# Optimization experiments

Hardware: AMD Instinct MI355X
Metric: run time of the kernel (lower is better)

## Reference

```python
import jax, jax.numpy as jnp
import numpy as np

B, S, H = 8, 4096, 1024
E, K = 64, 2
CAP_FACTOR = 1.25
TEMP = 1.0
LBW = 0.01


def setup_inputs() -> dict:
    key = jax.random.key(0)
    k1, k2, k3 = jax.random.split(key, 3)
    x = jax.random.normal(k1, (B, S, H), dtype=jnp.float32)
    gate_w = jax.random.normal(k2, (E, H), dtype=jnp.float32) * 0.02
    expert_w = jax.random.normal(k3, (E, H, H), dtype=jnp.float32) * 0.02
    return {"x": x, "gate_w": gate_w, "expert_w": expert_w}


def _moe_forward(x, gate_w, expert_w):
    b, s, h = x.shape
    xf = x.reshape(-1, h)                      # [N, H]
    N = xf.shape[0]
    capacity = int(N * K / E * CAP_FACTOR)

    # --- gating ---
    logits = xf @ gate_w.T                     # [N, E]
    vals, idx = jax.lax.top_k(logits / TEMP, K)  # [N, K]
    probs = jax.nn.softmax(vals, axis=-1)      # [N, K]

    # --- dispatch: first-come-first-served position within each expert ---
    ef = idx.reshape(-1)                       # [N*K], token-major order (matches torch loop)
    onehot = jax.nn.one_hot(ef, E, dtype=jnp.int32)            # [N*K, E]
    pos = jnp.take_along_axis(jnp.cumsum(onehot, axis=0), ef[:, None], axis=1)[:, 0] - 1
    valid = pos < capacity
    slot = jnp.where(valid, ef * capacity + pos, E * capacity)  # out-of-range -> dropped

    # token_map[e, c] = token_idx * K + k  (or -1 if empty)
    token_map = jnp.full((E * capacity,), -1, dtype=jnp.int32)
    token_map = token_map.at[slot].set(jnp.arange(N * K, dtype=jnp.int32), mode="drop")

    tok = jnp.clip(token_map // K, 0, N - 1)
    filled = token_map >= 0
    expert_inputs = jnp.where(filled[:, None], xf[tok], 0.0)    # [E*cap, H]
    expert_inputs = expert_inputs.reshape(E, capacity, h)

    # --- grouped expert GEMM (no bias; zero rows stay zero) ---
    expert_outputs = jnp.einsum("ech,edh->ecd", expert_inputs, expert_w)  # [E, cap, H]

    # --- combine: weighted scatter-add back to tokens ---
    eo_flat = expert_outputs.reshape(E * capacity, h)
    wk = token_map % K
    weight = jnp.where(filled, probs[tok, jnp.clip(wk, 0, K - 1)], 0.0)
    out_idx = jnp.where(filled, tok, N)        # invalid -> dropped
    output = jnp.zeros((N, h), dtype=xf.dtype).at[out_idx].add(
        weight[:, None] * eo_flat, mode="drop")

    # --- aux load-balancing loss ---
    gate_probs = jax.nn.softmax(logits, axis=-1)
    usage = jnp.bincount(ef, length=E).astype(jnp.float32) / (N * K + 1e-9)
    importance = gate_probs.mean(axis=0)
    aux = jnp.sum(usage * importance) * E
    aux = jnp.minimum(aux * LBW, 1.0)

    return output.reshape(b, s, h), aux


def reference(x, gate_w, expert_w):
    return _moe_forward(x, gate_w, expert_w)
```

## Files before the change

kernel.cpp:

```cpp
#include <hip/hip_runtime.h>
#include <hip/hip_bf16.h>

#define NTOK 32768
#define NE 64
#define HD 1024
#define CAP 1280
#define NKF (NTOK*2)
#define NSLOT (NE*CAP)
#define NTILE 128

typedef __attribute__((ext_vector_type(8))) short bf16x8;
typedef __attribute__((ext_vector_type(4))) short bf16x4;
typedef __attribute__((ext_vector_type(4))) float f32x4;
typedef __attribute__((ext_vector_type(4))) unsigned short u16x4;

__device__ __hip_bfloat16 g_zero[1152];

__device__ __forceinline__ short f2bf(float f) {
  union { __hip_bfloat16 b; short s; } u;
  u.b = __float2bfloat16(f);
  return u.s;
}
__device__ __forceinline__ float bf2f(unsigned short h) {
  return __uint_as_float(((unsigned)h) << 16);
}

__global__ __launch_bounds__(256, 4) void gating_kernel(const float* __restrict__ x,
                                                        const float* __restrict__ gw,
                                                        float* __restrict__ logits,
                                                        __hip_bfloat16* __restrict__ xb,
                                                        const float* __restrict__ ew,
                                                        __hip_bfloat16* __restrict__ wb) {
  __shared__ float Xs[64][66];
  __shared__ float Gs[64][66];
  const int tid = threadIdx.x;
  const int tok0 = blockIdx.x * 64;
  const int th = tid >> 4;
  const int te = tid & 15;
  float acc[4][4];
#pragma unroll
  for (int i = 0; i < 4; ++i)
#pragma unroll
    for (int j = 0; j < 4; ++j) acc[i][j] = 0.f;

  size_t ci = ((size_t)blockIdx.x * 256 + tid) * 8;
  const size_t cstride = (size_t)512 * 256 * 8;

  for (int k0i = 0; k0i < 16; ++k0i) {
    const int k0 = k0i * 64;
#pragma unroll
    for (int r = 0; r < 4; ++r) {
      int idx = r * 256 + tid;
      int row = idx >> 4;
      int c = (idx & 15) * 4;
      float4 xv4 = *(const float4*)&x[(size_t)(tok0 + row) * HD + k0 + c];
      *(float4*)&Xs[row][c] = xv4;
      bf16x4 o;
      o[0] = f2bf(xv4.x); o[1] = f2bf(xv4.y); o[2] = f2bf(xv4.z); o[3] = f2bf(xv4.w);
      *(bf16x4*)&xb[(size_t)(tok0 + row) * HD + k0 + c] = o;
      *(float4*)&Gs[row][c] = *(const float4*)&gw[(size_t)row * HD + k0 + c];
    }
    float4 ca[2], cb[2];
#pragma unroll
    for (int q = 0; q < 2; ++q) {
      ca[q] = *(const float4*)(ew + ci + (size_t)q * cstride);
      cb[q] = *(const float4*)(ew + ci + (size_t)q * cstride + 4);
    }
    __syncthreads();
#pragma unroll 4
    for (int kk = 0; kk < 8; ++kk) {
      float4 xv[4], gv[4];
#pragma unroll
      for (int i = 0; i < 4; ++i) xv[i] = *(float4*)&Xs[th + i * 16][kk * 4];
#pragma unroll
      for (int j = 0; j < 4; ++j) gv[j] = *(float4*)&Gs[te + j * 16][kk * 4];
#pragma unroll
      for (int i = 0; i < 4; ++i)
#pragma unroll
        for (int j = 0; j < 4; ++j) {
          acc[i][j] = fmaf(xv[i].x, gv[j].x, acc[i][j]);
          acc[i][j] = fmaf(xv[i].y, gv[j].y, acc[i][j]);
          acc[i][j] = fmaf(xv[i].z, gv[j].z, acc[i][j]);
          acc[i][j] = fmaf(xv[i].w, gv[j].w, acc[i][j]);
        }
    }
#pragma unroll
    for (int q = 0; q < 2; ++q) {
      bf16x8 o;
      o[0] = f2bf(ca[q].x); o[1] = f2bf(ca[q].y); o[2] = f2bf(ca[q].z); o[3] = f2bf(ca[q].w);
      o[4] = f2bf(cb[q].x); o[5] = f2bf(cb[q].y); o[6] = f2bf(cb[q].z); o[7] = f2bf(cb[q].w);
      *(bf16x8*)(wb + ci + (size_t)q * cstride) = o;
    }
#pragma unroll
    for (int q = 0; q < 2; ++q) {
      ca[q] = *(const float4*)(ew + ci + (size_t)(q + 2) * cstride);
      cb[q] = *(const float4*)(ew + ci + (size_t)(q + 2) * cstride + 4);
    }
#pragma unroll 4
    for (int kk = 8; kk < 16; ++kk) {
      float4 xv[4], gv[4];
#pragma unroll
      for (int i = 0; i < 4; ++i) xv[i] = *(float4*)&Xs[th + i * 16][kk * 4];
#pragma unroll
      for (int j = 0; j < 4; ++j) gv[j] = *(float4*)&Gs[te + j * 16][kk * 4];
#pragma unroll
      for (int i = 0; i < 4; ++i)
#pragma unroll
        for (int j = 0; j < 4; ++j) {
          acc[i][j] = fmaf(xv[i].x, gv[j].x, acc[i][j]);
          acc[i][j] = fmaf(xv[i].y, gv[j].y, acc[i][j]);
          acc[i][j] = fmaf(xv[i].z, gv[j].z, acc[i][j]);
          acc[i][j] = fmaf(xv[i].w, gv[j].w, acc[i][j]);
        }
    }
#pragma unroll
    for (int q = 0; q < 2; ++q) {
      bf16x8 o;
      o[0] = f2bf(ca[q].x); o[1] = f2bf(ca[q].y); o[2] = f2bf(ca[q].z); o[3] = f2bf(ca[q].w);
      o[4] = f2bf(cb[q].x); o[5] = f2bf(cb[q].y); o[6] = f2bf(cb[q].z); o[7] = f2bf(cb[q].w);
      *(bf16x8*)(wb + ci + (size_t)(q + 2) * cstride) = o;
    }
    ci += (size_t)4 * cstride;
    __syncthreads();
  }
#pragma unroll
  for (int i = 0; i < 4; ++i)
#pragma unroll
    for (int j = 0; j < 4; ++j)
      logits[(size_t)(tok0 + th + i * 16) * NE + te + j * 16] = acc[i][j];
}

__global__ __launch_bounds__(256) void topk_hist_kernel(const float* __restrict__ logits,
                                                        int2* __restrict__ e01,
                                                        float2* __restrict__ p01,
                                                        float* __restrict__ imp_part,
                                                        int* __restrict__ rank_buf,
                                                        int* __restrict__ hist) {
  __shared__ int wh[4][64];
  const int tid = threadIdx.x;
  const int w = tid >> 6, lane = tid & 63;
  const int t = blockIdx.x * 256 + tid;
  float l[64];
  const float4* lp = (const float4*)(logits + (size_t)t * NE);
#pragma unroll
  for (int i = 0; i < 16; ++i) {
    float4 v = lp[i];
    l[4 * i] = v.x; l[4 * i + 1] = v.y; l[4 * i + 2] = v.z; l[4 * i + 3] = v.w;
  }
  float v1 = -1e30f; int i1 = 0;
#pragma unroll
  for (int j = 0; j < 64; ++j) if (l[j] > v1) { v1 = l[j]; i1 = j; }
  float v2 = -1e30f; int i2 = 0;
#pragma unroll
  for (int j = 0; j < 64; ++j) if (j != i1 && l[j] > v2) { v2 = l[j]; i2 = j; }
  float ex = __expf(v2 - v1);
  float inv2 = 1.f / (1.f + ex);
  e01[t] = make_int2(i1, i2);
  p01[t] = make_float2(inv2, ex * inv2);

  float s = 0.f;
#pragma unroll
  for (int j = 0; j < 64; ++j) s += __expf(l[j] - v1);
  float invs = 1.f / s;
  const int wid = t >> 6;
#pragma unroll
  for (int e = 0; e < 64; ++e) {
    float p = __expf(l[e] - v1) * invs;
#pragma unroll
    for (int off = 32; off; off >>= 1) p += __shfl_xor(p, off);
    if (lane == 0) imp_part[(size_t)wid * 64 + e] = p;
  }

  int r0 = 0, r1 = 0, cnt = 0;
#pragma unroll
  for (int j = 0; j < 64; ++j) {
    int a = __shfl(i1, j);
    int b = __shfl(i2, j);
    int ja = (j < lane);
    r0 += ja & (a == i1);
    r0 += ja & (b == i1);
    r1 += ja & (a == i2);
    r1 += ja & (b == i2);
    cnt += (a == lane) + (b == lane);
  }
  wh[w][lane] = cnt;
  __syncthreads();
#pragma unroll
  for (int ww = 0; ww < 4; ++ww)
    if (ww < w) { r0 += wh[ww][i1]; r1 += wh[ww][i2]; }
  rank_buf[2 * t] = r0;
  rank_buf[2 * t + 1] = r1;
  if (tid < 64)
    hist[blockIdx.x * 64 + tid] = wh[0][tid] + wh[1][tid] + wh[2][tid] + wh[3][tid];
}

__global__ __launch_bounds__(64) void scan_aux_kernel(const int* __restrict__ hist,
                                                      const float* __restrict__ imp_part,
                                                      int* __restrict__ tile_off,
                                                      int* __restrict__ counts,
                                                      float* __restrict__ out) {
  const int e = threadIdx.x;
  int run = 0;
  for (int t = 0; t < NTILE; ++t) {
    int h = hist[t * 64 + e];
    tile_off[t * 64 + e] = run;
    run += h;
  }
  counts[e] = run;

  float imp = 0.f;
  for (int w = 0; w < 512; ++w) imp += imp_part[(size_t)w * 64 + e];
  imp *= (1.f / (float)NTOK);
  float usage = (float)run / (float)NKF;
  float v = usage * imp;
#pragma unroll
  for (int off = 32; off; off >>= 1) v += __shfl_xor(v, off);
  if (e == 0) out[(size_t)NTOK * HD] = fminf(v * (float)NE * 0.01f, 1.0f);
}

__global__ __launch_bounds__(256) void place_kernel(const int2* __restrict__ e01,
                                                    const int* __restrict__ rank_buf,
                                                    const int* __restrict__ tile_off,
                                                    int* __restrict__ slot_of,
                                                    int* __restrict__ slot_token) {
  const int tid = threadIdx.x;
  const int i = blockIdx.x * 256 + tid;
  int2 ee = e01[i >> 1];
  const int e = (i & 1) ? ee.y : ee.x;
  const int pos = tile_off[(i >> 9) * 64 + e] + rank_buf[i];
  const int slot = (pos < CAP) ? (e * CAP + pos) : -1;
  slot_of[i] = slot;
  if (slot >= 0) slot_token[slot] = i;
}

#define ASYNC16(g, l) __builtin_amdgcn_global_load_lds( \
    (const __attribute__((address_space(1))) void*)(g), \
    (__attribute__((address_space(3))) void*)(l), 16, 0, 0)

#define STAGE_A(buf, ks, kcol) do {                                             \
    const int _d = ((buf) * 16384 + (ks) * 8192 + wuni) * 2;                    \
    ASYNC16(arow0 + (kcol) + (ks) * 32 + sw8, (char*)lds + _d);                 \
    ASYNC16(arow1 + (kcol) + (ks) * 32 + sw8, (char*)lds + _d + 8192);          \
  } while (0)

#define STAGE_B3(buf3, ks, kcol) do {                                           \
    const __hip_bfloat16* _g = B + (size_t)srow * HD + (kcol) + (ks) * 32 + sw8; \
    const int _d = (32768 + (buf3) * 16384 + (ks) * 8192 + wuni) * 2;           \
    ASYNC16(_g, (char*)lds + _d);                                               \
    ASYNC16(_g + (size_t)128 * HD, (char*)lds + _d + 8192);                     \
  } while (0)

#define LDA(dst, buf, ks, mi) \
  dst = *(const bf16x8*)(lds + (buf) * 16384 + (ks) * 8192 + (wm * 128 + (mi) * 16 + fr) * 32 + rsw)
#define LDB3(dst, buf3, ks, ni) \
  dst = *(const bf16x8*)(lds + 32768 + (buf3) * 16384 + (ks) * 8192 + (wn * 64 + (ni) * 16 + fr) * 32 + rsw)

#define MFMA_HALF(h)                                                            \
  _Pragma("unroll")                                                             \
  for (int mm = 0; mm < 4; ++mm)                                                \
    _Pragma("unroll")                                                           \
    for (int nn = 0; nn < 4; ++nn)                                              \
      acc[(h) * 4 + mm][nn] =                                                   \
          __builtin_amdgcn_mfma_f32_16x16x32_bf16(av[mm], bv[nn], acc[(h) * 4 + mm][nn], 0, 0, 0)

#define BARX() do { asm volatile("" ::: "memory"); __builtin_amdgcn_s_barrier(); asm volatile("" ::: "memory"); } while (0)
#define VMC(n) asm volatile("s_waitcnt vmcnt(" #n ")" ::: "memory")

__global__ __launch_bounds__(512, 2) void moe_gemm_kernel(const __hip_bfloat16* __restrict__ xb,
                                                          const int* __restrict__ slot_token,
                                                          const __hip_bfloat16* __restrict__ Wb,
                                                          const int* __restrict__ counts,
                                                          __hip_bfloat16* __restrict__ Eo) {
  __shared__ __hip_bfloat16 lds[81920];

  const int bid = blockIdx.x;
  const int swz = (bid & 7) * 160 + (bid >> 3);
  const int e = swz / 20;
  const int t20 = swz - e * 20;
  const int tm = t20 >> 2, tn = t20 & 3;

  const int cnt = counts[e];
  if (tm * 256 >= cnt) return;

  const int tid = threadIdx.x;
  const int lane = tid & 63;
  const int w = tid >> 6;
  const int wm = w >> 2, wn = w & 3;

  const __hip_bfloat16* B = Wb + (size_t)e * HD * HD + (size_t)(tn * 256) * HD;

  const int srow = tid >> 2;
  const int sw8 = ((tid & 3) ^ ((tid >> 3) & 3)) * 8;
  const int wuni = w * 512;

  const int slotbase = e * CAP + tm * 256;
  const int r0row = tm * 256 + srow;
  const int i0 = slot_token[slotbase + srow];
  const int i1 = slot_token[slotbase + 128 + srow];
  const __hip_bfloat16* arow0 = (r0row < cnt) ? xb + (size_t)(i0 >> 1) * HD : g_zero;
  const __hip_bfloat16* arow1 = (r0row + 128 < cnt) ? xb + (size_t)(i1 >> 1) * HD : g_zero;

  const int fr = lane & 15;
  const int fq = lane >> 4;
  const int rsw = (fq ^ ((fr >> 1) & 3)) * 8;

  f32x4 acc[8][4] = {};

  STAGE_A(0, 0, 0);
  STAGE_A(0, 1, 0);
  STAGE_B3(0, 0, 0);
  STAGE_B3(0, 1, 0);
  STAGE_B3(1, 0, 64);
  STAGE_B3(1, 1, 64);
  VMC(4);
  BARX();

#pragma unroll 2
  for (int t = 0; t < 16; ++t) {
    const int ard = t & 1, ast = ard ^ 1;
    const int b_rd = t % 3;
    int b_st = b_rd + 2; if (b_st >= 3) b_st -= 3;
    const int kcA = (t + 1) * 64;
    const int kcB = (t + 2) * 64;
    const bool hA = (t < 15);
    const bool hB = (t < 14);
    bf16x8 av[4], bv[4];

    LDB3(bv[0], b_rd, 0, 0); LDB3(bv[1], b_rd, 0, 1); LDB3(bv[2], b_rd, 0, 2); LDB3(bv[3], b_rd, 0, 3);
    LDA(av[0], ard, 0, 0); LDA(av[1], ard, 0, 1); LDA(av[2], ard, 0, 2); LDA(av[3], ard, 0, 3);
    if (hA) STAGE_A(ast, 0, kcA);
    BARX();
    __builtin_amdgcn_s_setprio(1);
    MFMA_HALF(0);
    __builtin_amdgcn_s_setprio(0);
    BARX();

    LDA(av[0], ard, 0, 4); LDA(av[1], ard, 0, 5); LDA(av[2], ard, 0, 6); LDA(av[3], ard, 0, 7);
    if (hB) {
      STAGE_B3(b_st, 0, kcB);
      VMC(6);
    } else if (t == 14) {
      VMC(4);
    } else {
      VMC(0);
    }
    BARX();
    __builtin_amdgcn_s_setprio(1);
    MFMA_HALF(1);
    __builtin_amdgcn_s_setprio(0);
    BARX();

    LDB3(bv[0], b_rd, 1, 0); LDB3(bv[1], b_rd, 1, 1); LDB3(bv[2], b_rd, 1, 2); LDB3(bv[3], b_rd, 1, 3);
    LDA(av[0], ard, 1, 0); LDA(av[1], ard, 1, 1); LDA(av[2], ard, 1, 2); LDA(av[3], ard, 1, 3);
    if (hA) STAGE_A(ast, 1, kcA);
    BARX();
    __builtin_amdgcn_s_setprio(1);
    MFMA_HALF(0);
    __builtin_amdgcn_s_setprio(0);
    BARX();

    LDA(av[0], ard, 1, 4); LDA(av[1], ard, 1, 5); LDA(av[2], ard, 1, 6); LDA(av[3], ard, 1, 7);
    if (hB) {
      STAGE_B3(b_st, 1, kcB);
      VMC(6);
    } else if (t == 14) {
      VMC(2);
    }
    BARX();
    __builtin_amdgcn_s_setprio(1);
    MFMA_HALF(1);
    __builtin_amdgcn_s_setprio(0);
    BARX();
  }

  __hip_bfloat16* C = Eo + (size_t)e * CAP * HD +
                      (size_t)(tm * 256 + wm * 128) * HD + tn * 256 + wn * 64;
#pragma unroll
  for (int m = 0; m < 8; ++m)
#pragma unroll
    for (int n = 0; n < 4; ++n)
#pragma unroll
      for (int r = 0; r < 4; ++r)
        C[(size_t)(m * 16 + fq * 4 + r) * HD + n * 16 + fr] = __float2bfloat16(acc[m][n][r]);
}

__global__ __launch_bounds__(256) void combine_kernel(const __hip_bfloat16* __restrict__ eo,
                                                      const int* __restrict__ slot_of,
                                                      const float2* __restrict__ p01,
                                                      float* __restrict__ out) {
  const int t = blockIdx.x;
  const int tid = threadIdx.x;
  const float2 p = p01[t];
  const int s0 = slot_of[2 * t], s1 = slot_of[2 * t + 1];
  float a0 = 0.f, a1 = 0.f, a2 = 0.f, a3 = 0.f;
  if (s0 >= 0) {
    u16x4 v = *(const u16x4*)((const unsigned short*)eo + (size_t)s0 * HD + tid * 4);
    a0 += p.x * bf2f(v[0]); a1 += p.x * bf2f(v[1]);
    a2 += p.x * bf2f(v[2]); a3 += p.x * bf2f(v[3]);
  }
  if (s1 >= 0) {
    u16x4 v = *(const u16x4*)((const unsigned short*)eo + (size_t)s1 * HD + tid * 4);
    a0 += p.y * bf2f(v[0]); a1 += p.y * bf2f(v[1]);
    a2 += p.y * bf2f(v[2]); a3 += p.y * bf2f(v[3]);
  }
  float4 res = make_float4(a0, a1, a2, a3);
  *(float4*)(out + (size_t)t * HD + tid * 4) = res;
}

extern "C" void kernel_launch(void* const* d_in, const int* in_sizes, int n_in,
                              void* d_out, int out_size, void* d_ws, size_t ws_size,
                              hipStream_t stream) {
  const float* x = (const float*)d_in[0];
  const float* gw = (const float*)d_in[1];
  const float* ew = (const float*)d_in[2];
  float* out = (float*)d_out;

  char* p = (char*)d_ws;
  float* logits = (float*)p;            p += (size_t)NTOK * NE * 4;
  int2* e01 = (int2*)p;                 p += (size_t)NTOK * 8;
  float2* p01 = (float2*)p;             p += (size_t)NTOK * 8;
  int* slot_of = (int*)p;               p += (size_t)NKF * 4;
  int* slot_token = (int*)p;            p += (size_t)NSLOT * 4;
  int* counts = (int*)p;                p += 256;
  float* imp_part = (float*)p;          p += (size_t)512 * 64 * 4;
  int* rank_buf = (int*)p;              p += (size_t)NKF * 4;
  int* hist = (int*)p;                  p += (size_t)NTILE * 64 * 4;
  int* tile_off = (int*)p;              p += (size_t)NTILE * 64 * 4;
  __hip_bfloat16* xb = (__hip_bfloat16*)p; p += (size_t)NTOK * HD * 2;
  __hip_bfloat16* Wb = (__hip_bfloat16*)p;  p += (size_t)NE * HD * HD * 2;
  __hip_bfloat16* Eo = (__hip_bfloat16*)p;  p += (size_t)NSLOT * HD * 2;

  gating_kernel<<<NTOK / 64, 256, 0, stream>>>(x, gw, logits, xb, ew, Wb);
  topk_hist_kernel<<<NTOK / 256, 256, 0, stream>>>(logits, e01, p01, imp_part, rank_buf, hist);
  scan_aux_kernel<<<1, 64, 0, stream>>>(hist, imp_part, tile_off, counts, out);
  place_kernel<<<NKF / 256, 256, 0, stream>>>(e01, rank_buf, tile_off, slot_of, slot_token);
  moe_gemm_kernel<<<dim3(1280), 512, 0, stream>>>(xb, slot_token, Wb, counts, Eo);
  combine_kernel<<<NTOK, 256, 0, stream>>>(Eo, slot_of, p01, out);
}
```

Before: 405.5 us.

## Fuse top-k softmax and importance into gating kernel epilogue

Moves the top-2 selection, routing probabilities and per-block importance sums into the gating kernel's epilogue, reading logits from shared memory instead of writing and re-reading an 8 MB logits buffer. The remaining hist/rank kernel now reads only e01. imp_part is now indexed per 64-token block, which matches the old per-wavefront layout. Only 64 of 256 threads do the epilogue work, which adds serial tail time to each gating block.

Measured after the change: 393.0 us. -3.1%, faster.

```diff
diff --git a/kernel.cpp b/kernel.cpp
--- a/kernel.cpp
+++ b/kernel.cpp
@@ -27,12 +27,15 @@
 
 __global__ __launch_bounds__(256, 4) void gating_kernel(const float* __restrict__ x,
                                                         const float* __restrict__ gw,
-                                                        float* __restrict__ logits,
                                                         __hip_bfloat16* __restrict__ xb,
                                                         const float* __restrict__ ew,
-                                                        __hip_bfloat16* __restrict__ wb) {
+                                                        __hip_bfloat16* __restrict__ wb,
+                                                        int2* __restrict__ e01,
+                                                        float2* __restrict__ p01,
+                                                        float* __restrict__ imp_part) {
   __shared__ float Xs[64][66];
   __shared__ float Gs[64][66];
+  __shared__ float v1s[64], invss[64];
   const int tid = threadIdx.x;
   const int tok0 = blockIdx.x * 64;
   const int th = tid >> 4;
@@ -123,54 +126,49 @@
     ci += (size_t)4 * cstride;
     __syncthreads();
   }
+
+  float (*Ls)[66] = Xs;
 #pragma unroll
   for (int i = 0; i < 4; ++i)
 #pragma unroll
     for (int j = 0; j < 4; ++j)
-      logits[(size_t)(tok0 + th + i * 16) * NE + te + j * 16] = acc[i][j];
-}
-
-__global__ __launch_bounds__(256) void topk_hist_kernel(const float* __restrict__ logits,
-                                                        int2* __restrict__ e01,
-                                                        float2* __restrict__ p01,
-                                                        float* __restrict__ imp_part,
+      Ls[th + i * 16][te + j * 16] = acc[i][j];
+  __syncthreads();
+  if (tid < 64) {
+    float v1 = -1e30f; int i1 = 0;
+#pragma unroll
+    for (int j = 0; j < 64; ++j) { float lv = Ls[tid][j]; if (lv > v1) { v1 = lv; i1 = j; } }
+    float v2 = -1e30f; int i2 = 0;
+#pragma unroll
+    for (int j = 0; j < 64; ++j) { float lv = Ls[tid][j]; if (j != i1 && lv > v2) { v2 = lv; i2 = j; } }
+    float ex = __expf(v2 - v1);
+    float inv2 = 1.f / (1.f + ex);
+    e01[tok0 + tid] = make_int2(i1, i2);
+    p01[tok0 + tid] = make_float2(inv2, ex * inv2);
+    float s = 0.f;
+#pragma unroll
+    for (int j = 0; j < 64; ++j) s += __expf(Ls[tid][j] - v1);
+    v1s[tid] = v1;
+    invss[tid] = 1.f / s;
+  }
+  __syncthreads();
+  if (tid < 64) {
+    float imp = 0.f;
+#pragma unroll
+    for (int t2 = 0; t2 < 64; ++t2) imp += __expf(Ls[t2][tid] - v1s[t2]) * invss[t2];
+    imp_part[(size_t)blockIdx.x * 64 + tid] = imp;
+  }
+}
+
+__global__ __launch_bounds__(256) void hist_rank_kernel(const int2* __restrict__ e01,
                                                         int* __restrict__ rank_buf,
                                                         int* __restrict__ hist) {
   __shared__ int wh[4][64];
   const int tid = threadIdx.x;
   const int w = tid >> 6, lane = tid & 63;
   const int t = blockIdx.x * 256 + tid;
-  float l[64];
-  const float4* lp = (const float4*)(logits + (size_t)t * NE);
-#pragma unroll
-  for (int i = 0; i < 16; ++i) {
-    float4 v = lp[i];
-    l[4 * i] = v.x; l[4 * i + 1] = v.y; l[4 * i + 2] = v.z; l[4 * i + 3] = v.w;
-  }
-  float v1 = -1e30f; int i1 = 0;
-#pragma unroll
-  for (int j = 0; j < 64; ++j) if (l[j] > v1) { v1 = l[j]; i1 = j; }
-  float v2 = -1e30f; int i2 = 0;
-#pragma unroll
-  for (int j = 0; j < 64; ++j) if (j != i1 && l[j] > v2) { v2 = l[j]; i2 = j; }
-  float ex = __expf(v2 - v1);
-  float inv2 = 1.f / (1.f + ex);
-  e01[t] = make_int2(i1, i2);
-  p01[t] = make_float2(inv2, ex * inv2);
-
-  float s = 0.f;
-#pragma unroll
-  for (int j = 0; j < 64; ++j) s += __expf(l[j] - v1);
-  float invs = 1.f / s;
-  const int wid = t >> 6;
-#pragma unroll
-  for (int e = 0; e < 64; ++e) {
-    float p = __expf(l[e] - v1) * invs;
-#pragma unroll
-    for (int off = 32; off; off >>= 1) p += __shfl_xor(p, off);
-    if (lane == 0) imp_part[(size_t)wid * 64 + e] = p;
-  }
-
+  int2 ee = e01[t];
+  const int i1 = ee.x, i2 = ee.y;
   int r0 = 0, r1 = 0, cnt = 0;
 #pragma unroll
   for (int j = 0; j < 64; ++j) {
@@ -416,7 +414,6 @@
   float* out = (float*)d_out;
 
   char* p = (char*)d_ws;
-  float* logits = (float*)p;            p += (size_t)NTOK * NE * 4;
   int2* e01 = (int2*)p;                 p += (size_t)NTOK * 8;
   float2* p01 = (float2*)p;             p += (size_t)NTOK * 8;
   int* slot_of = (int*)p;               p += (size_t)NKF * 4;
@@ -430,8 +427,8 @@
   __hip_bfloat16* Wb = (__hip_bfloat16*)p;  p += (size_t)NE * HD * HD * 2;
   __hip_bfloat16* Eo = (__hip_bfloat16*)p;  p += (size_t)NSLOT * HD * 2;
 
-  gating_kernel<<<NTOK / 64, 256, 0, stream>>>(x, gw, logits, xb, ew, Wb);
-  topk_hist_kernel<<<NTOK / 256, 256, 0, stream>>>(logits, e01, p01, imp_part, rank_buf, hist);
+  gating_kernel<<<NTOK / 64, 256, 0, stream>>>(x, gw, xb, ew, Wb, e01, p01, imp_part);
+  hist_rank_kernel<<<NTOK / 256, 256, 0, stream>>>(e01, rank_buf, hist);
   scan_aux_kernel<<<1, 64, 0, stream>>>(hist, imp_part, tile_off, counts, out);
   place_kernel<<<NKF / 256, 256, 0, stream>>>(e01, rank_buf, tile_off, slot_of, slot_token);
   moe_gemm_kernel<<<dim3(1280), 512, 0, stream>>>(xb, slot_token, Wb, counts, Eo);
```
